# Performance work log

Measured on AMD Instinct MI355X. Metric: run time of the kernel, lower is better.

## Reference

```python
import jax, jax.numpy as jnp
import numpy as np

N = 50000      # nodes
E = 800000     # edges
IN, HID, OUT = 256, 256, 128
FCH = 32       # fc_hidden per embedding
VDIM = 2
FINAL = 2
NUM_EMB = 20


def setup_inputs() -> dict:
    key = jax.random.key(0)
    ks = jax.random.split(key, 16)
    s = 0.05
    return {
        "x": jax.random.normal(ks[0], (N, IN), jnp.float32),
        "edge_index": jax.random.randint(ks[1], (2, E), 0, N),
        "edge_cat": jax.random.randint(ks[2], (E, 2), 0, NUM_EMB),
        "edge_val": jax.random.normal(ks[3], (E, VDIM), jnp.float32),
        "W1": jax.random.normal(ks[4], (IN, HID), jnp.float32) * s,
        "b1": jnp.zeros((HID,), jnp.float32),
        "W2": jax.random.normal(ks[5], (HID, OUT), jnp.float32) * s,
        "b2": jnp.zeros((OUT,), jnp.float32),
        "emb0": jax.random.normal(ks[6], (NUM_EMB, FCH), jnp.float32) * s,
        "emb1": jax.random.normal(ks[7], (NUM_EMB, FCH), jnp.float32) * s,
        "fW1": jax.random.normal(ks[8], (OUT + 2 * FCH + VDIM, FINAL), jnp.float32) * s,
        "fb1": jnp.zeros((FINAL,), jnp.float32),
        "fW2": jax.random.normal(ks[9], (FINAL, 2), jnp.float32) * s,
        "fb2": jnp.zeros((2,), jnp.float32),
    }


def gcn_conv(h_in, W, b, src, dst, n):
    # PyG GCNConv: linear, add self-loops, symmetric D^-1/2 (A+I) D^-1/2 aggregation, bias.
    h = h_in @ W                                    # [N, F]
    ones = jnp.ones(src.shape[0], h.dtype)
    deg = jax.ops.segment_sum(ones, dst, num_segments=n) + 1.0  # +1 self-loop
    dinv = jax.lax.rsqrt(deg)                       # deg >= 1 so finite
    norm = dinv[src] * dinv[dst]                    # [E]
    agg = jax.ops.segment_sum(h[src] * norm[:, None], dst, num_segments=n)
    agg = agg + h * (dinv * dinv)[:, None]          # self-loop term, norm = dinv_i^2
    return agg + b


def reference(x, edge_index, edge_cat, edge_val,
              W1, b1, W2, b2, emb0, emb1, fW1, fb1, fW2, fb2):
    src, dst = edge_index[0], edge_index[1]
    n = x.shape[0]
    h = jax.nn.relu(gcn_conv(x, W1, b1, src, dst, n))
    h = gcn_conv(h, W2, b2, src, dst, n)            # [N, OUT]
    node2edge = h[src] - h[dst]                     # [E, OUT]
    ev = jnp.concatenate([edge_val, emb0[edge_cat[:, 0]], emb1[edge_cat[:, 1]]], axis=1)
    total = jnp.concatenate([node2edge, ev], axis=1)  # [E, OUT+2*FCH+VDIM]
    z = jax.nn.relu(total @ fW1 + fb1)              # dropout is identity in eval mode
    return z @ fW2 + fb2                            # [E, 2]
```

## Files before the change

kernel.cpp:

```cpp
#include <hip/hip_runtime.h>

#define NN 50000
#define XPAD 50048
#define EE 800000
#define NB ((NN + 1023) / 1024)
#define DEGB ((EE + 255) / 256)
#define NCVT (XPAD / 16)
#define GEMMB (XPAD / 64)
#define FILLB ((EE + 511) / 512)

typedef _Float16 half8v __attribute__((ext_vector_type(8)));
typedef _Float16 half4v __attribute__((ext_vector_type(4)));
typedef float f32x4 __attribute__((ext_vector_type(4)));

__device__ __forceinline__ void gload16(const _Float16* g, _Float16* l) {
    __builtin_amdgcn_global_load_lds(
        (const __attribute__((address_space(1))) unsigned int*)g,
        (__attribute__((address_space(3))) unsigned int*)l, 16, 0, 0);
}

__global__ __launch_bounds__(256) void deg_prep(const int* __restrict__ dst,
                                                int* __restrict__ deg,
                                                int* __restrict__ epos,
                                                const float* __restrict__ x,
                                                _Float16* __restrict__ xh,
                                                const float* __restrict__ W1,
                                                const float* __restrict__ W2,
                                                const float* __restrict__ fW1,
                                                const float* __restrict__ emb0,
                                                const float* __restrict__ emb1,
                                                _Float16* __restrict__ BT,
                                                float* __restrict__ Wft,
                                                float2* __restrict__ t0,
                                                float2* __restrict__ t1) {
    __shared__ float T[64][65];
    int b = blockIdx.x;
    int t = threadIdx.x;
    if (b < DEGB) {
        int e = b * 256 + t;
        if (e < EE) epos[e] = atomicAdd(&deg[dst[e]], 1);
    } else if (b < DEGB + NCVT) {
        int b2 = b - DEGB;
        int row = b2 * 16 + (t >> 4);
        int col = (t & 15) * 16;
        half8v h0, h1;
        if (row < NN) {
            const float4* xp = (const float4*)&x[(size_t)row * 256 + col];
            float4 v0 = xp[0], v1 = xp[1], v2 = xp[2], v3 = xp[3];
            h0[0] = (_Float16)v0.x; h0[1] = (_Float16)v0.y;
            h0[2] = (_Float16)v0.z; h0[3] = (_Float16)v0.w;
            h0[4] = (_Float16)v1.x; h0[5] = (_Float16)v1.y;
            h0[6] = (_Float16)v1.z; h0[7] = (_Float16)v1.w;
            h1[0] = (_Float16)v2.x; h1[1] = (_Float16)v2.y;
            h1[2] = (_Float16)v2.z; h1[3] = (_Float16)v2.w;
            h1[4] = (_Float16)v3.x; h1[5] = (_Float16)v3.y;
            h1[6] = (_Float16)v3.z; h1[7] = (_Float16)v3.w;
        } else {
            h0 = (half8v)(_Float16)0.f;
            h1 = (half8v)(_Float16)0.f;
        }
        *(half8v*)&xh[(size_t)row * 256 + col] = h0;
        *(half8v*)&xh[(size_t)row * 256 + col + 8] = h1;
    } else if (b < DEGB + NCVT + 16) {
        int bb = b - DEGB - NCVT;
        int k0 = (bb >> 2) * 64, n0 = (bb & 3) * 64;
#pragma unroll
        for (int i = 0; i < 16; ++i) {
            int r = i * 4 + (t >> 6), c = t & 63;
            T[r][c] = W1[(size_t)(k0 + r) * 256 + n0 + c];
        }
        __syncthreads();
#pragma unroll
        for (int i = 0; i < 16; ++i) {
            int n = i * 4 + (t >> 6), k = t & 63;
            BT[(size_t)(n0 + n) * 256 + k0 + k] = (_Float16)T[k][n];
        }
    } else {
        int k = t;
        float s0 = 0.f, s1 = 0.f;
        for (int m = 0; m < 128; ++m) {
            float wv = W2[(size_t)k * 128 + m];
            s0 += wv * fW1[m * 2 + 0];
            s1 += wv * fW1[m * 2 + 1];
        }
        Wft[k] = s0;
        Wft[256 + k] = s1;
        if (k < 20) {
            float a0 = 0.f, a1 = 0.f, b0 = 0.f, b1v = 0.f;
            for (int u = 0; u < 32; ++u) {
                float e0 = emb0[k * 32 + u], e1 = emb1[k * 32 + u];
                a0 += e0 * fW1[(130 + u) * 2 + 0];
                a1 += e0 * fW1[(130 + u) * 2 + 1];
                b0 += e1 * fW1[(162 + u) * 2 + 0];
                b1v += e1 * fW1[(162 + u) * 2 + 1];
            }
            t0[k] = make_float2(a0, a1);
            t1[k] = make_float2(b0, b1v);
        }
    }
}

__global__ __launch_bounds__(1024) void scan_partial(const int* __restrict__ deg,
                                                     int* __restrict__ rowptr,
                                                     int* __restrict__ bsum) {
    __shared__ int wsum[16];
    int tid = threadIdx.x, lane = tid & 63, w = tid >> 6;
    int idx = blockIdx.x * 1024 + tid;
    int v = (idx < NN) ? deg[idx] : 0;
    int x = v;
#pragma unroll
    for (int off = 1; off < 64; off <<= 1) {
        int t = __shfl_up(x, off, 64);
        if (lane >= off) x += t;
    }
    if (lane == 63) wsum[w] = x;
    __syncthreads();
    if (w == 0) {
        int s = (lane < 16) ? wsum[lane] : 0;
#pragma unroll
        for (int off = 1; off < 16; off <<= 1) {
            int t = __shfl_up(s, off, 64);
            if (lane >= off) s += t;
        }
        if (lane < 16) wsum[lane] = s;
    }
    __syncthreads();
    int wpre = (w == 0) ? 0 : wsum[w - 1];
    if (idx < NN) rowptr[idx] = wpre + (x - v);
    if (tid == 0) bsum[blockIdx.x] = wsum[15];
}

__global__ __launch_bounds__(256) void scan_add_dinv(int* __restrict__ rowptr,
                                                     const int* __restrict__ bsum,
                                                     const int* __restrict__ deg,
                                                     float* __restrict__ dinv) {
    __shared__ int pre[NB + 1];
    int t = threadIdx.x;
    if (t < 64) {
        int v = (t < NB) ? bsum[t] : 0;
        int x = v;
#pragma unroll
        for (int o = 1; o < 64; o <<= 1) {
            int y = __shfl_up(x, o, 64);
            if (t >= o) x += y;
        }
        if (t < NB) pre[t] = x - v;
        if (t == NB - 1) pre[NB] = x;
    }
    __syncthreads();
    int idx = blockIdx.x * 256 + t;
    if (idx < NN) {
        rowptr[idx] += pre[idx >> 10];
        dinv[idx] = rsqrtf((float)deg[idx] + 1.0f);
    }
    if (blockIdx.x == 0 && t == 0) rowptr[NN] = pre[NB];
}

__global__ __launch_bounds__(512) void gemm_fill(const _Float16* __restrict__ Axh,
                                                 const _Float16* __restrict__ BT,
                                                 _Float16* __restrict__ C, int M,
                                                 const int* __restrict__ src,
                                                 const int* __restrict__ dst,
                                                 const int* __restrict__ rowptr,
                                                 const int* __restrict__ epos,
                                                 int* __restrict__ csr_src) {
    if (blockIdx.x >= GEMMB) {
        int e = (blockIdx.x - GEMMB) * 512 + threadIdx.x;
        if (e < EE) {
            int d = dst[e];
            csr_src[rowptr[d] + epos[e]] = src[e];
        }
        return;
    }
    __shared__ _Float16 Ah[2][64 * 32];
    __shared__ _Float16 Bh[2][256 * 32];
    int tid = threadIdx.x;
    int bm = blockIdx.x * 64;
    int w = tid >> 6, l = tid & 63;
    int wr = w >> 2, wc = w & 3;
    int lr = l & 15, lg = l >> 4;
    f32x4 acc[2][4] = {};

    const _Float16* gA  = Axh + (size_t)(bm + (tid >> 2)) * 256 + (tid & 3) * 8;
    const _Float16* gB0 = BT + (size_t)(tid >> 2) * 256 + (tid & 3) * 8;
    const _Float16* gB1 = BT + (size_t)((tid >> 2) + 128) * 256 + (tid & 3) * 8;

    auto stage = [&](int buf, int k0) {
        if (tid < 256) gload16(gA + k0, &Ah[buf][tid * 8]);
        gload16(gB0 + k0, &Bh[buf][tid * 8]);
        gload16(gB1 + k0, &Bh[buf][(tid + 512) * 8]);
    };

    stage(0, 0);
    __syncthreads();
#pragma unroll
    for (int ks = 0; ks < 8; ++ks) {
        int cur = ks & 1;
        if (ks < 7) stage(cur ^ 1, (ks + 1) * 32);
        half8v a[2], b[4];
#pragma unroll
        for (int mf = 0; mf < 2; ++mf)
            a[mf] = *(const half8v*)&Ah[cur][(wr * 32 + mf * 16 + lr) * 32 + lg * 8];
#pragma unroll
        for (int nf = 0; nf < 4; ++nf)
            b[nf] = *(const half8v*)&Bh[cur][(wc * 64 + nf * 16 + lr) * 32 + lg * 8];
#pragma unroll
        for (int mf = 0; mf < 2; ++mf)
#pragma unroll
            for (int nf = 0; nf < 4; ++nf)
                acc[mf][nf] = __builtin_amdgcn_mfma_f32_16x16x32_f16(a[mf], b[nf], acc[mf][nf], 0, 0, 0);
        __syncthreads();
    }
#pragma unroll
    for (int mf = 0; mf < 2; ++mf) {
#pragma unroll
        for (int reg = 0; reg < 4; ++reg) {
            int gr = bm + wr * 32 + mf * 16 + lg * 4 + reg;
            if (gr < M) {
#pragma unroll
                for (int nf = 0; nf < 4; ++nf)
                    C[(size_t)gr * 256 + wc * 64 + nf * 16 + lr] =
                        (_Float16)acc[mf][nf][reg];
            }
        }
    }
}

__global__ __launch_bounds__(256) void gather_project(const _Float16* __restrict__ hs,
                                                      const int* __restrict__ rowptr,
                                                      const int* __restrict__ csr_src,
                                                      const float* __restrict__ dinv,
                                                      const float* __restrict__ b1,
                                                      const float* __restrict__ Wft,
                                                      float2* __restrict__ q) {
    int i = blockIdx.x * 4 + (threadIdx.x >> 6);
    int l = threadIdx.x & 63;
    int lf = l & 31, le = l >> 5;
    if (i >= NN) return;
    int start = rowptr[i], end = rowptr[i + 1];
    float acc[8] = {};
    int j = start;
    for (; j + 7 < end; j += 8) {
        int s0 = csr_src[j + 0 + le];
        int s1 = csr_src[j + 2 + le];
        int s2 = csr_src[j + 4 + le];
        int s3 = csr_src[j + 6 + le];
        float d0 = dinv[s0], d1 = dinv[s1], d2 = dinv[s2], d3 = dinv[s3];
        half8v v0 = *(const half8v*)(hs + (size_t)s0 * 256 + lf * 8);
        half8v v1 = *(const half8v*)(hs + (size_t)s1 * 256 + lf * 8);
        half8v v2 = *(const half8v*)(hs + (size_t)s2 * 256 + lf * 8);
        half8v v3 = *(const half8v*)(hs + (size_t)s3 * 256 + lf * 8);
#pragma unroll
        for (int u = 0; u < 8; ++u)
            acc[u] += (d0 * (float)v0[u] + d1 * (float)v1[u]) +
                      (d2 * (float)v2[u] + d3 * (float)v3[u]);
    }
    for (; j + le < end; j += 2) {
        int s = csr_src[j + le];
        float ds = dinv[s];
        half8v v = *(const half8v*)(hs + (size_t)s * 256 + lf * 8);
#pragma unroll
        for (int u = 0; u < 8; ++u) acc[u] += ds * (float)v[u];
    }
#pragma unroll
    for (int u = 0; u < 8; ++u) acc[u] += __shfl_xor(acc[u], 32, 64);
    float di = dinv[i];
    half8v sv = *(const half8v*)(hs + (size_t)i * 256 + lf * 8);
    float q0 = 0.f, q1 = 0.f;
#pragma unroll
    for (int u = 0; u < 8; ++u) {
        float o = fmaxf((acc[u] + di * (float)sv[u]) * di + b1[lf * 8 + u], 0.f);
        q0 += o * Wft[lf * 8 + u];
        q1 += o * Wft[256 + lf * 8 + u];
    }
#pragma unroll
    for (int off = 16; off > 0; off >>= 1) {
        q0 += __shfl_xor(q0, off, 64);
        q1 += __shfl_xor(q1, off, 64);
    }
    if (l == 0) q[i] = make_float2(q0 * di, q1 * di);
}

__global__ __launch_bounds__(256) void gather_gn(const float2* __restrict__ q,
                                                 const int* __restrict__ rowptr,
                                                 const int* __restrict__ csr_src,
                                                 const float* __restrict__ dinv,
                                                 float2* __restrict__ gn) {
    int i = blockIdx.x * blockDim.x + threadIdx.x;
    if (i >= NN) return;
    int start = rowptr[i], end = rowptr[i + 1];
    float a0 = 0.f, a1 = 0.f;
    for (int j = start; j < end; ++j) {
        float2 v = q[csr_src[j]];
        a0 += v.x;
        a1 += v.y;
    }
    float2 self = q[i];
    float di = dinv[i];
    gn[i] = make_float2((a0 + self.x) * di, (a1 + self.y) * di);
}

__global__ __launch_bounds__(256) void edge_out(const float2* __restrict__ gn,
                                                const int* __restrict__ src,
                                                const int* __restrict__ dst,
                                                const int2* __restrict__ ecat,
                                                const float2* __restrict__ ev,
                                                const float* __restrict__ fW1,
                                                const float2* __restrict__ t0,
                                                const float2* __restrict__ t1,
                                                const float* __restrict__ fb1,
                                                const float* __restrict__ fW2,
                                                const float* __restrict__ fb2,
                                                float2* __restrict__ out) {
    int e = blockIdx.x * blockDim.x + threadIdx.x;
    if (e >= EE) return;
    int s = src[e], d = dst[e];
    float2 gs = gn[s], gd = gn[d];
    int2 c = ecat[e];
    float2 v = ev[e];
    float2 e0 = t0[c.x], e1 = t1[c.y];
    float z0 = gs.x - gd.x + v.x * fW1[128 * 2 + 0] + v.y * fW1[129 * 2 + 0] + e0.x + e1.x;
    float z1 = gs.y - gd.y + v.x * fW1[128 * 2 + 1] + v.y * fW1[129 * 2 + 1] + e0.y + e1.y;
    float y0 = fmaxf(z0 + fb1[0], 0.f);
    float y1 = fmaxf(z1 + fb1[1], 0.f);
    out[e] = make_float2(y0 * fW2[0] + y1 * fW2[2] + fb2[0],
                         y0 * fW2[1] + y1 * fW2[3] + fb2[1]);
}

extern "C" void kernel_launch(void* const* d_in, const int* in_sizes, int n_in,
                              void* d_out, int out_size, void* d_ws, size_t ws_size,
                              hipStream_t stream) {
    const float* x    = (const float*)d_in[0];
    const int*   eidx = (const int*)d_in[1];
    const int*   src  = eidx;
    const int*   dst  = eidx + EE;
    const int*   ecat = (const int*)d_in[2];
    const float* ev   = (const float*)d_in[3];
    const float* W1   = (const float*)d_in[4];
    const float* b1   = (const float*)d_in[5];
    const float* W2   = (const float*)d_in[6];
    const float* emb0 = (const float*)d_in[8];
    const float* emb1 = (const float*)d_in[9];
    const float* fW1  = (const float*)d_in[10];
    const float* fb1  = (const float*)d_in[11];
    const float* fW2  = (const float*)d_in[12];
    const float* fb2  = (const float*)d_in[13];
    float* out = (float*)d_out;

    char* ws = (char*)d_ws;
    size_t off = 0;
    auto alloc = [&](size_t bytes) {
        void* p = ws + off;
        off = (off + bytes + 255) & ~(size_t)255;
        return p;
    };
    int*      deg     = (int*)alloc((size_t)NN * 4);
    float*    dinv    = (float*)alloc((size_t)NN * 4);
    int*      rowptr  = (int*)alloc((size_t)(NN + 1) * 4);
    int*      bsum    = (int*)alloc((size_t)NB * 4);
    int*      epos    = (int*)alloc((size_t)EE * 4);
    int*      csr_src = (int*)alloc((size_t)EE * 4);
    _Float16* W1T     = (_Float16*)alloc((size_t)256 * 256 * 2);
    _Float16* xh      = (_Float16*)alloc((size_t)XPAD * 256 * 2);
    _Float16* h1s     = (_Float16*)alloc((size_t)NN * 256 * 2);
    float2*   q       = (float2*)alloc((size_t)NN * 8);
    float2*   gn      = (float2*)alloc((size_t)NN * 8);
    float*    Wft     = (float*)alloc(512 * 4);
    float2*   t0      = (float2*)alloc(20 * 8);
    float2*   t1      = (float2*)alloc(20 * 8);

    hipMemsetAsync(deg, 0, (size_t)NN * 4, stream);

    deg_prep<<<DEGB + NCVT + 17, 256, 0, stream>>>(dst, deg, epos, x, xh,
                                                   W1, W2, fW1, emb0, emb1,
                                                   W1T, Wft, t0, t1);

    scan_partial<<<NB, 1024, 0, stream>>>(deg, rowptr, bsum);
    scan_add_dinv<<<(NN + 255) / 256, 256, 0, stream>>>(rowptr, bsum, deg, dinv);

    gemm_fill<<<GEMMB + FILLB, 512, 0, stream>>>(xh, W1T, h1s, NN,
                                                 src, dst, rowptr, epos, csr_src);

    gather_project<<<(NN + 3) / 4, 256, 0, stream>>>(
        h1s, rowptr, csr_src, dinv, b1, Wft, q);
    gather_gn<<<(NN + 255) / 256, 256, 0, stream>>>(q, rowptr, csr_src, dinv, gn);
    edge_out<<<DEGB, 256, 0, stream>>>(
        gn, src, dst, (const int2*)ecat, (const float2*)ev,
        fW1, t0, t1, fb1, fW2, fb2, (float2*)out);
}
```

Before: 164.0 us.

## Fuse fp32-to-fp16 conversion of x into the GEMM A-tile load

Drops the separate pass that converted x to a padded fp16 buffer. The GEMM now streams fp32 rows of x straight into LDS and converts to fp16 in registers before the MFMA, clamping out-of-range rows instead of padding. This removes one full write and re-read of an N×256 half buffer, at the cost of twice the LDS bytes for A tiles and conversion work in the inner loop. The gather_project launch is also split into two half-range launches on the same stream, which adds launch overhead without any obvious benefit.

```diff
diff --git a/kernel.cpp b/kernel.cpp
--- a/kernel.cpp
+++ b/kernel.cpp
@@ -1,19 +1,16 @@
 #include <hip/hip_runtime.h>
 
 #define NN 50000
-#define XPAD 50048
 #define EE 800000
 #define NB ((NN + 1023) / 1024)
 #define DEGB ((EE + 255) / 256)
-#define NCVT (XPAD / 16)
-#define GEMMB (XPAD / 64)
+#define GEMMB ((NN + 63) / 64)
 #define FILLB ((EE + 511) / 512)
 
 typedef _Float16 half8v __attribute__((ext_vector_type(8)));
-typedef _Float16 half4v __attribute__((ext_vector_type(4)));
 typedef float f32x4 __attribute__((ext_vector_type(4)));
 
-__device__ __forceinline__ void gload16(const _Float16* g, _Float16* l) {
+__device__ __forceinline__ void gload16(const void* g, void* l) {
     __builtin_amdgcn_global_load_lds(
         (const __attribute__((address_space(1))) unsigned int*)g,
         (__attribute__((address_space(3))) unsigned int*)l, 16, 0, 0);
@@ -22,8 +19,6 @@
 __global__ __launch_bounds__(256) void deg_prep(const int* __restrict__ dst,
                                                 int* __restrict__ deg,
                                                 int* __restrict__ epos,
-                                                const float* __restrict__ x,
-                                                _Float16* __restrict__ xh,
                                                 const float* __restrict__ W1,
                                                 const float* __restrict__ W2,
                                                 const float* __restrict__ fW1,
@@ -39,30 +34,8 @@
     if (b < DEGB) {
         int e = b * 256 + t;
         if (e < EE) epos[e] = atomicAdd(&deg[dst[e]], 1);
-    } else if (b < DEGB + NCVT) {
-        int b2 = b - DEGB;
-        int row = b2 * 16 + (t >> 4);
-        int col = (t & 15) * 16;
-        half8v h0, h1;
-        if (row < NN) {
-            const float4* xp = (const float4*)&x[(size_t)row * 256 + col];
-            float4 v0 = xp[0], v1 = xp[1], v2 = xp[2], v3 = xp[3];
-            h0[0] = (_Float16)v0.x; h0[1] = (_Float16)v0.y;
-            h0[2] = (_Float16)v0.z; h0[3] = (_Float16)v0.w;
-            h0[4] = (_Float16)v1.x; h0[5] = (_Float16)v1.y;
-            h0[6] = (_Float16)v1.z; h0[7] = (_Float16)v1.w;
-            h1[0] = (_Float16)v2.x; h1[1] = (_Float16)v2.y;
-            h1[2] = (_Float16)v2.z; h1[3] = (_Float16)v2.w;
-            h1[4] = (_Float16)v3.x; h1[5] = (_Float16)v3.y;
-            h1[6] = (_Float16)v3.z; h1[7] = (_Float16)v3.w;
-        } else {
-            h0 = (half8v)(_Float16)0.f;
-            h1 = (half8v)(_Float16)0.f;
-        }
-        *(half8v*)&xh[(size_t)row * 256 + col] = h0;
-        *(half8v*)&xh[(size_t)row * 256 + col + 8] = h1;
-    } else if (b < DEGB + NCVT + 16) {
-        int bb = b - DEGB - NCVT;
+    } else if (b < DEGB + 16) {
+        int bb = b - DEGB;
         int k0 = (bb >> 2) * 64, n0 = (bb & 3) * 64;
 #pragma unroll
         for (int i = 0; i < 16; ++i) {
@@ -156,7 +129,7 @@
     if (blockIdx.x == 0 && t == 0) rowptr[NN] = pre[NB];
 }
 
-__global__ __launch_bounds__(512) void gemm_fill(const _Float16* __restrict__ Axh,
+__global__ __launch_bounds__(512) void gemm_fill(const float* __restrict__ A,
                                                  const _Float16* __restrict__ BT,
                                                  _Float16* __restrict__ C, int M,
                                                  const int* __restrict__ src,
@@ -172,7 +145,7 @@
         }
         return;
     }
-    __shared__ _Float16 Ah[2][64 * 32];
+    __shared__ float    Ahf[2][2048];
     __shared__ _Float16 Bh[2][256 * 32];
     int tid = threadIdx.x;
     int bm = blockIdx.x * 64;
@@ -181,12 +154,14 @@
     int lr = l & 15, lg = l >> 4;
     f32x4 acc[2][4] = {};
 
-    const _Float16* gA  = Axh + (size_t)(bm + (tid >> 2)) * 256 + (tid & 3) * 8;
+    int ar = tid & 63, aq = tid >> 6;
+    int garow = bm + ar; if (garow >= M) garow = M - 1;
+    const float* gA = A + (size_t)garow * 256 + aq * 4;
     const _Float16* gB0 = BT + (size_t)(tid >> 2) * 256 + (tid & 3) * 8;
     const _Float16* gB1 = BT + (size_t)((tid >> 2) + 128) * 256 + (tid & 3) * 8;
 
     auto stage = [&](int buf, int k0) {
-        if (tid < 256) gload16(gA + k0, &Ah[buf][tid * 8]);
+        gload16(gA + k0, &Ahf[buf][tid * 4]);
         gload16(gB0 + k0, &Bh[buf][tid * 8]);
         gload16(gB1 + k0, &Bh[buf][(tid + 512) * 8]);
     };
@@ -199,8 +174,18 @@
         if (ks < 7) stage(cur ^ 1, (ks + 1) * 32);
         half8v a[2], b[4];
 #pragma unroll
-        for (int mf = 0; mf < 2; ++mf)
-            a[mf] = *(const half8v*)&Ah[cur][(wr * 32 + mf * 16 + lr) * 32 + lg * 8];
+        for (int mf = 0; mf < 2; ++mf) {
+            int r = wr * 32 + mf * 16 + lr;
+            int q0 = 2 * lg;
+            f32x4 va = *(const f32x4*)&Ahf[cur][(q0 * 64 + r) * 4];
+            f32x4 vb = *(const f32x4*)&Ahf[cur][((q0 + 1) * 64 + r) * 4];
+            half8v h;
+            h[0] = (_Float16)va[0]; h[1] = (_Float16)va[1];
+            h[2] = (_Float16)va[2]; h[3] = (_Float16)va[3];
+            h[4] = (_Float16)vb[0]; h[5] = (_Float16)vb[1];
+            h[6] = (_Float16)vb[2]; h[7] = (_Float16)vb[3];
+            a[mf] = h;
+        }
 #pragma unroll
         for (int nf = 0; nf < 4; ++nf)
             b[nf] = *(const half8v*)&Bh[cur][(wc * 64 + nf * 16 + lr) * 32 + lg * 8];
@@ -232,11 +217,12 @@
                                                       const float* __restrict__ dinv,
                                                       const float* __restrict__ b1,
                                                       const float* __restrict__ Wft,
-                                                      float2* __restrict__ q) {
-    int i = blockIdx.x * 4 + (threadIdx.x >> 6);
+                                                      float2* __restrict__ q,
+                                                      int base, int cnt) {
+    int i = base + blockIdx.x * 4 + (threadIdx.x >> 6);
     int l = threadIdx.x & 63;
     int lf = l & 31, le = l >> 5;
-    if (i >= NN) return;
+    if (i >= base + cnt || i >= NN) return;
     int start = rowptr[i], end = rowptr[i + 1];
     float acc[8] = {};
     int j = start;
@@ -361,7 +347,6 @@
     int*      epos    = (int*)alloc((size_t)EE * 4);
     int*      csr_src = (int*)alloc((size_t)EE * 4);
     _Float16* W1T     = (_Float16*)alloc((size_t)256 * 256 * 2);
-    _Float16* xh      = (_Float16*)alloc((size_t)XPAD * 256 * 2);
     _Float16* h1s     = (_Float16*)alloc((size_t)NN * 256 * 2);
     float2*   q       = (float2*)alloc((size_t)NN * 8);
     float2*   gn      = (float2*)alloc((size_t)NN * 8);
@@ -371,18 +356,24 @@
 
     hipMemsetAsync(deg, 0, (size_t)NN * 4, stream);
 
-    deg_prep<<<DEGB + NCVT + 17, 256, 0, stream>>>(dst, deg, epos, x, xh,
-                                                   W1, W2, fW1, emb0, emb1,
-                                                   W1T, Wft, t0, t1);
+    deg_prep<<<DEGB + 17, 256, 0, stream>>>(dst, deg, epos,
+                                            W1, W2, fW1, emb0, emb1,
+                                            W1T, Wft, t0, t1);
 
     scan_partial<<<NB, 1024, 0, stream>>>(deg, rowptr, bsum);
     scan_add_dinv<<<(NN + 255) / 256, 256, 0, stream>>>(rowptr, bsum, deg, dinv);
 
-    gemm_fill<<<GEMMB + FILLB, 512, 0, stream>>>(xh, W1T, h1s, NN,
+    gemm_fill<<<GEMMB + FILLB, 512, 0, stream>>>(x, W1T, h1s, NN,
                                                  src, dst, rowptr, epos, csr_src);
 
-    gather_project<<<(NN + 3) / 4, 256, 0, stream>>>(
-        h1s, rowptr, csr_src, dinv, b1, Wft, q);
+    {
+        int half1 = NN / 2;
+        int half2 = NN - half1;
+        gather_project<<<(half1 + 3) / 4, 256, 0, stream>>>(
+            h1s, rowptr, csr_src, dinv, b1, Wft, q, 0, half1);
+        gather_project<<<(half2 + 3) / 4, 256, 0, stream>>>(
+            h1s, rowptr, csr_src, dinv, b1, Wft, q, half1, half2);
+    }
     gather_gn<<<(NN + 255) / 256, 256, 0, stream>>>(q, rowptr, csr_src, dinv, gn);
     edge_out<<<DEGB, 256, 0, stream>>>(
         gn, src, dst, (const int2*)ecat, (const float2*)ev,
```

After: 166.2 us. About the same (+1.4%).
